# Optimization experiments

Measured on AMD Instinct MI355X. Metric: run time of the kernel, lower is better.

Reference implementation:

```python
import jax, jax.numpy as jnp
import numpy as np
from jax import lax

C_DIM = 64
N_HEADS = 8
PATCH = 3
PAD = (PATCH - 1) // 2
EPS = 1e-6


def _unfold(x, p, pad):
    # x: [B,C,H,W] -> [B, C*p*p, H*W], torch.F.unfold ordering (C slowest, then ph, pw)
    B, C, H, W = x.shape
    xp = jnp.pad(x, ((0, 0), (0, 0), (pad, pad), (pad, pad)))
    cols = jnp.stack([xp[:, :, i:i + H, j:j + W] for i in range(p) for j in range(p)], axis=2)
    return cols.reshape(B, C * p * p, H * W)


def _fold(cols, p, pad, H, W):
    # cols: [B, C*p*p, H*W] -> [B,C,H,W] via col2im scatter-add (torch.F.fold)
    B = cols.shape[0]
    C = cols.shape[1] // (p * p)
    cols = cols.reshape(B, C, p * p, H, W)
    out = jnp.zeros((B, C, H + 2 * pad, W + 2 * pad), cols.dtype)
    for i in range(p):
        for j in range(p):
            out = out.at[:, :, i:i + H, j:j + W].add(cols[:, :, i * p + j])
    return out[:, :, pad:pad + H, pad:pad + W]


def _linear_attn(q, k, v):
    # q,k,v: [B, h, N, d]; non-softmax linear attention with ReLU features
    kv = jnp.einsum('bhnd,bhne->bhde', k, v)          # [B,h,d,d]
    ksum = k.sum(axis=2)                              # [B,h,d]
    denom = jnp.einsum('bhnd,bhd->bhn', q, ksum) + EPS
    out = jnp.einsum('bhnd,bhde->bhne', q, kv) / denom[..., None]
    return out


def setup_inputs() -> dict:
    key = jax.random.key(0)
    ks = jax.random.split(key, 5)
    B, C, H, W = 4, C_DIM, 128, 128
    x = jax.random.normal(ks[0], (B, C, H, W), jnp.float32)
    w_qkv = jax.random.normal(ks[1], (3 * C, C), jnp.float32) * 0.05
    b_qkv = jax.random.normal(ks[2], (3 * C,), jnp.float32) * 0.01
    w_proj = jax.random.normal(ks[3], (C, C, 3, 3), jnp.float32) * 0.05
    b_proj = jax.random.normal(ks[4], (C,), jnp.float32) * 0.01
    return {"x": x, "w_qkv": w_qkv, "b_qkv": b_qkv, "w_proj": w_proj, "b_proj": b_proj}


def reference(x, w_qkv, b_qkv, w_proj, b_proj):
    B, C, H, W = x.shape
    p, pad, h = PATCH, PAD, N_HEADS
    N = H * W
    # 1x1 conv qkv
    qkv = jnp.einsum('bchw,oc->bohw', x, w_qkv) + b_qkv[None, :, None, None]
    q, k, v = qkv[:, :C], qkv[:, C:2 * C], qkv[:, 2 * C:]
    q = jax.nn.relu(q)
    k = jax.nn.relu(k)
    # im2col: [B, C*p*p, N]
    qc = _unfold(q, p, pad)
    kc = _unfold(k, p, pad)
    vc = _unfold(v, p, pad)
    d = (C * p * p) // h
    qh = qc.reshape(B, h, d, N).transpose(0, 1, 3, 2)  # [B,h,N,d]
    kh = kc.reshape(B, h, d, N).transpose(0, 1, 3, 2)
    vh = vc.reshape(B, h, d, N).transpose(0, 1, 3, 2)
    o = _linear_attn(qh, kh, vh)                       # [B,h,N,d]
    oc = o.transpose(0, 1, 3, 2).reshape(B, C * p * p, N)
    folded = _fold(oc, p, pad, H, W)
    ones_cols = _unfold(jnp.ones((B, C, H, W), x.dtype), p, pad)
    counts = _fold(ones_cols, p, pad, H, W)
    y = folded / counts
    # 3x3 proj conv
    y = lax.conv_general_dilated(y, w_proj, (1, 1), [(1, 1), (1, 1)],
                                 dimension_numbers=('NCHW', 'OIHW', 'NCHW'))
    y = y + b_proj[None, :, None, None]
    return y
```

## Files before the change

kernel.cpp:

```cpp
#include <hip/hip_runtime.h>

#define BB 4
#define CC 64
#define HH 128
#define WW 128
#define NN (HH*WW)
#define HP 130
#define NPP (HP*HP)
#define HP2 132
#define NPP2 (HP2*HP2)
#define NH 8
#define DD 72

__global__ __launch_bounds__(256) void k0_wt(const float* __restrict__ wproj, float* __restrict__ wt){
    int idx = blockIdx.x*256 + threadIdx.x;
    if (idx >= 64*9*64) return;
    int oc = idx & 63;
    int w  = (idx >> 6) % 9;
    int ci = idx / 576;
    wt[idx] = wproj[(oc*64 + ci)*9 + w];
}

__global__ __launch_bounds__(256) void k1_qkv(const float* __restrict__ x,
        const float* __restrict__ wqkv, const float* __restrict__ bqkv,
        float* __restrict__ Qp, float* __restrict__ Kp, float* __restrict__ Vp){
    __shared__ float wl[64*68];
    __shared__ float bl[64];
    const int t = threadIdx.x;
    const int gy = blockIdx.y;
    const int b  = blockIdx.z;
    for (int k = 0; k < 16; ++k){
        int idx = t + k*256;
        int orel = idx >> 6, c = idx & 63;
        wl[c*68 + orel] = wqkv[(gy*64 + orel)*64 + c];
    }
    if (t < 64) bl[t] = bqkv[gy*64 + t];
    __syncthreads();
    const int pix = blockIdx.x*256 + t;
    float acc[64];
#pragma unroll
    for (int o=0;o<64;++o) acc[o]=0.f;
    const float* xb = x + (size_t)(b*64)*NN + pix;
    for (int c=0;c<64;++c){
        float xv = xb[(size_t)c*NN];
        const float4* wrow = (const float4*)(&wl[c*68]);
#pragma unroll
        for (int o4=0;o4<16;++o4){
            float4 wv = wrow[o4];
            acc[o4*4+0] += xv*wv.x;
            acc[o4*4+1] += xv*wv.y;
            acc[o4*4+2] += xv*wv.z;
            acc[o4*4+3] += xv*wv.w;
        }
    }
    const int y = pix >> 7, xx = pix & 127;
    float* dst; size_t cstride;
    if (gy == 0){ dst = Qp + (size_t)(b*64)*NPP2 + (y+2)*HP2 + (xx+2); cstride = NPP2; }
    else { dst = ((gy==1)?Kp:Vp) + (size_t)(b*64)*NPP + (y+1)*HP + (xx+1); cstride = NPP; }
    const bool dorelu = (gy < 2);
#pragma unroll
    for (int o=0;o<64;++o){
        float v = acc[o] + bl[o];
        if (dorelu) v = fmaxf(v, 0.f);
        dst[(size_t)o*cstride] = v;
    }
}

__global__ __launch_bounds__(256) void k2_ksum(const float* __restrict__ Kp, float* __restrict__ ksum){
    const int c = blockIdx.x, b = blockIdx.y;
    const float* src = Kp + (size_t)(b*64 + c)*NPP;
    float a[3][3];
#pragma unroll
    for (int i=0;i<3;++i)
#pragma unroll
        for (int j=0;j<3;++j) a[i][j]=0.f;
    for (int idx = threadIdx.x; idx < NPP; idx += 256){
        int r = idx / HP, cc = idx - r*HP;
        float v = src[idx];
#pragma unroll
        for (int i=0;i<3;++i){
            bool fy = (unsigned)(r - i) < 128u;
#pragma unroll
            for (int j=0;j<3;++j){
                bool fx = (unsigned)(cc - j) < 128u;
                if (fy && fx) a[i][j] += v;
            }
        }
    }
    __shared__ float red[4][9];
#pragma unroll
    for (int i=0;i<3;++i)
#pragma unroll
        for (int j=0;j<3;++j){
            float v = a[i][j];
            for (int m=1;m<64;m<<=1) v += __shfl_xor(v, m, 64);
            a[i][j] = v;
        }
    int wave = threadIdx.x >> 6, lane = threadIdx.x & 63;
    if (lane == 0){
#pragma unroll
        for (int w=0;w<9;++w) red[wave][w] = a[w/3][w%3];
    }
    __syncthreads();
    if (threadIdx.x < 9){
        float s = red[0][threadIdx.x]+red[1][threadIdx.x]+red[2][threadIdx.x]+red[3][threadIdx.x];
        int h = c >> 3, cl = c & 7;
        ksum[(b*NH + h)*DD + cl*9 + threadIdx.x] = s;
    }
}

__global__ __launch_bounds__(256) void k3_kv(const float* __restrict__ Kp, const float* __restrict__ Vp,
                                             float* __restrict__ kvT2){
    const int cc2 = blockIdx.x;
    const int cd = cc2 >> 3, ce = cc2 & 7;
    const int h = blockIdx.y, b = blockIdx.z;
    const float* Kc = Kp + (size_t)(b*64 + h*8 + cd)*NPP;
    const float* Vc = Vp + (size_t)(b*64 + h*8 + ce)*NPP;
    float acc[9][9];
#pragma unroll
    for (int i=0;i<9;++i)
#pragma unroll
        for (int j=0;j<9;++j) acc[i][j]=0.f;
    for (int it=0; it<64; ++it){
        int pix = threadIdx.x + it*256;
        int y = pix >> 7, xx = pix & 127;
        const float* kb = Kc + y*HP + xx;
        const float* vb = Vc + y*HP + xx;
        float kw[9], vw[9];
#pragma unroll
        for (int w=0;w<9;++w){ kw[w] = kb[(w/3)*HP + (w%3)]; vw[w] = vb[(w/3)*HP + (w%3)]; }
#pragma unroll
        for (int w=0;w<9;++w)
#pragma unroll
            for (int w2=0;w2<9;++w2) acc[w][w2] += kw[w]*vw[w2];
    }
    __shared__ float red[4][81];
#pragma unroll
    for (int w=0;w<9;++w)
#pragma unroll
        for (int w2=0;w2<9;++w2){
            float v = acc[w][w2];
            for (int m=1;m<64;m<<=1) v += __shfl_xor(v, m, 64);
            acc[w][w2] = v;
        }
    int wave = threadIdx.x >> 6, lane = threadIdx.x & 63;
    if (lane == 0){
#pragma unroll
        for (int w=0;w<9;++w)
#pragma unroll
            for (int w2=0;w2<9;++w2) red[wave][w*9+w2] = acc[w][w2];
    }
    __syncthreads();
    if (threadIdx.x < 81){
        float s = red[0][threadIdx.x]+red[1][threadIdx.x]+red[2][threadIdx.x]+red[3][threadIdx.x];
        int w = threadIdx.x / 9, w2 = threadIdx.x - w*9;
        kvT2[((size_t)(b*NH + h)*DD + ce*9 + w2)*96 + cd*12 + w] = s;
    }
}

__global__ __launch_bounds__(256) void k4_r(const float* __restrict__ Qp, const float* __restrict__ ksum,
                                            float* __restrict__ rfp){
    const int h = blockIdx.y, b = blockIdx.z;
    __shared__ float ks[72];
    if (threadIdx.x < 72) ks[threadIdx.x] = ksum[(b*NH + h)*DD + threadIdx.x];
    __syncthreads();
    const int pix = blockIdx.x*256 + threadIdx.x;
    const int y = pix >> 7, xx = pix & 127;
    const float* Qb = Qp + (size_t)(b*64 + h*8)*NPP2 + (y+1)*HP2 + (xx+1);
    float denom = 0.f;
#pragma unroll
    for (int cl=0; cl<8; ++cl){
        const float* q = Qb + (size_t)cl*NPP2;
#pragma unroll
        for (int w=0; w<9; ++w){
            denom += q[(w/3)*HP2 + (w%3)] * ks[cl*9 + w];
        }
    }
    rfp[(size_t)(b*NH + h)*NPP + (y+1)*HP + (xx+1)] = 1.f/(denom + 1e-6f);
}

__global__ __launch_bounds__(512) void k5_attn(const float* __restrict__ Qp, const float* __restrict__ kvT2,
          const float* __restrict__ rfp, float* __restrict__ folded){
    __shared__ __align__(16) float Qt[8*20*20];
    __shared__ __align__(16) float rt[18*20];
    const int t = threadIdx.x;
    const int tile = blockIdx.x;
    const int h = blockIdx.y, b = blockIdx.z;
    const int ty0 = (tile >> 3)*16, tx0 = (tile & 7)*16;

    const float* Qb = Qp + (size_t)(b*64 + h*8)*NPP2 + (size_t)ty0*HP2 + tx0;
    for (int idx=t; idx<8*20*20; idx+=512){
        int cl = idx / 400; int rem = idx - cl*400; int r = rem/20, cc = rem - r*20;
        Qt[idx] = Qb[(size_t)cl*NPP2 + r*HP2 + cc];
    }
    const float* rg = rfp + (size_t)(b*NH + h)*NPP + (size_t)ty0*HP + tx0;
    for (int idx=t; idx<18*18; idx+=512){
        int rr = idx / 18, cc = idx - rr*18;
        rt[rr*20 + cc] = rg[rr*HP + cc];
    }
    __syncthreads();

    const int c  = __builtin_amdgcn_readfirstlane(t >> 6);
    const int l  = t & 63;
    const int pr = l >> 2;
    const int pc = (l & 3) * 4;

    const float* kvc = kvT2 + ((size_t)(b*NH + h)*DD + c*9)*96;

    float acc[9][4];
#pragma unroll
    for (int u=0;u<9;++u)
#pragma unroll
        for (int p=0;p<4;++p) acc[u][p]=0.f;

    for (int cl=0; cl<8; ++cl){
        float qw[5][8];
        const float* qb = &Qt[cl*400 + pr*20 + pc];
#pragma unroll
        for (int rr=0; rr<5; ++rr){
            float4 a0 = *(const float4*)(qb + rr*20);
            float4 a1 = *(const float4*)(qb + rr*20 + 4);
            qw[rr][0]=a0.x; qw[rr][1]=a0.y; qw[rr][2]=a0.z; qw[rr][3]=a0.w;
            qw[rr][4]=a1.x; qw[rr][5]=a1.y; qw[rr][6]=a1.z; qw[rr][7]=a1.w;
        }
#pragma unroll
        for (int u=0; u<9; ++u){
            const float* kr = kvc + u*96 + cl*12;
            float kw[9];
#pragma unroll
            for (int i=0;i<9;++i) kw[i] = kr[i];
            const int iu = u/3, ju = u - iu*3;
#pragma unroll
            for (int w=0; w<9; ++w){
                const int rr = (w/3) - iu + 2;
                const int cc = (w%3) - ju + 2;
#pragma unroll
                for (int p=0;p<4;++p)
                    acc[u][p] += qw[rr][cc+p] * kw[w];
            }
        }
    }
    float rw[3][6];
    const float* rb = &rt[pr*20 + pc];
#pragma unroll
    for (int rr=0; rr<3; ++rr)
#pragma unroll
        for (int j=0; j<6; ++j) rw[rr][j] = rb[rr*20 + j];
    float out[4];
#pragma unroll
    for (int p=0;p<4;++p) out[p]=0.f;
#pragma unroll
    for (int u=0; u<9; ++u){
        const int iu = u/3, ju = u - iu*3;
#pragma unroll
        for (int p=0;p<4;++p)
            out[p] += acc[u][p] * rw[2-iu][p+2-ju];
    }
    float4 o4 = make_float4(out[0], out[1], out[2], out[3]);
    *(float4*)(&folded[(size_t)(b*64 + h*8 + c)*NN + (ty0+pr)*WW + tx0 + pc]) = o4;
}

__global__ __launch_bounds__(256) void k6_conv(const float* __restrict__ folded, const float* __restrict__ wt,
         const float* __restrict__ bproj, float* __restrict__ out){
    __shared__ __align__(16) float ut[8*18*12];
    const int t = threadIdx.x;
    const int tile = blockIdx.x;
    const int b = blockIdx.y;
    const int ty0 = (tile >> 4)*16, tx0 = (tile & 15)*8;
    const int ocb = t & 15;
    const int s   = t >> 4;
    float acc[4][8];
#pragma unroll
    for (int ol=0;ol<4;++ol)
#pragma unroll
        for (int p=0;p<8;++p) acc[ol][p]=0.f;
    const float4 bias = *(const float4*)(&bproj[ocb*4]);

    for (int ch=0; ch<8; ++ch){
        __syncthreads();
        for (int idx=t; idx<8*18*10; idx+=256){
            int cil = idx / 180; int rem = idx - cil*180; int rr = rem/10, cc = rem - rr*10;
            int iy = ty0 - 1 + rr, ix = tx0 - 1 + cc;
            float v = 0.f;
            if ((unsigned)iy < 128u && (unsigned)ix < 128u){
                int ry = 3 - (iy==0) - (iy==127);
                int rx = 3 - (ix==0) - (ix==127);
                v = folded[(size_t)(b*64 + ch*8 + cil)*NN + iy*WW + ix] / (float)(ry*rx);
            }
            ut[cil*216 + rr*12 + cc] = v;
        }
        __syncthreads();
        for (int cil=0; cil<8; ++cil){
            const int ci = ch*8 + cil;
            float uw[3][10];
            const float* ub = &ut[cil*216 + s*12];
#pragma unroll
            for (int dy=0;dy<3;++dy){
                float4 a0 = *(const float4*)(ub + dy*12);
                float4 a1 = *(const float4*)(ub + dy*12 + 4);
                float2 a2 = *(const float2*)(ub + dy*12 + 8);
                uw[dy][0]=a0.x; uw[dy][1]=a0.y; uw[dy][2]=a0.z; uw[dy][3]=a0.w;
                uw[dy][4]=a1.x; uw[dy][5]=a1.y; uw[dy][6]=a1.z; uw[dy][7]=a1.w;
                uw[dy][8]=a2.x; uw[dy][9]=a2.y;
            }
#pragma unroll
            for (int w=0;w<9;++w){
                const int dy = w/3, dx = w%3;
                float4 wv = *(const float4*)(&wt[(ci*9 + w)*64 + ocb*4]);
#pragma unroll
                for (int p=0;p<8;++p){
                    float u = uw[dy][p+dx];
                    acc[0][p] += wv.x*u;
                    acc[1][p] += wv.y*u;
                    acc[2][p] += wv.z*u;
                    acc[3][p] += wv.w*u;
                }
            }
        }
    }
    const int y = ty0 + s;
#pragma unroll
    for (int ol=0;ol<4;++ol){
        const int oc = ocb*4 + ol;
        float* dst = &out[(size_t)(b*64 + oc)*NN + y*WW + tx0];
        float bv = (ol==0)?bias.x:(ol==1)?bias.y:(ol==2)?bias.z:bias.w;
#pragma unroll
        for (int p=0;p<8;++p) dst[p] = acc[ol][p] + bv;
    }
}

extern "C" void kernel_launch(void* const* d_in, const int* in_sizes, int n_in,
                              void* d_out, int out_size, void* d_ws, size_t ws_size,
                              hipStream_t stream) {
    const float* x     = (const float*)d_in[0];
    const float* wqkv  = (const float*)d_in[1];
    const float* bqkv  = (const float*)d_in[2];
    const float* wproj = (const float*)d_in[3];
    const float* bproj = (const float*)d_in[4];
    float* out = (float*)d_out;
    float* ws  = (float*)d_ws;

    const size_t szQ2 = (size_t)BB*CC*NPP2;
    const size_t szF  = (size_t)BB*CC*NPP;
    const size_t szR  = (size_t)BB*NH*NPP;
    float* Qp2    = ws;
    float* Kp     = Qp2 + szQ2;
    float* Vp     = Kp + szF;
    float* rfp    = Vp + szF;
    float* folded = rfp + szR;
    float* kvT2   = folded + (size_t)BB*CC*NN;
    float* ksum   = kvT2 + (size_t)BB*NH*DD*96;
    float* wt     = ksum + (size_t)BB*NH*DD;

    hipMemsetAsync(ws, 0, (szQ2 + 2*szF + szR)*sizeof(float), stream);

    k0_wt  <<<dim3(144),      256, 0, stream>>>(wproj, wt);
    k1_qkv <<<dim3(64, 3, 4), 256, 0, stream>>>(x, wqkv, bqkv, Qp2, Kp, Vp);
    k2_ksum<<<dim3(64, 4),    256, 0, stream>>>(Kp, ksum);
    k3_kv  <<<dim3(64, 8, 4), 256, 0, stream>>>(Kp, Vp, kvT2);
    k4_r   <<<dim3(64, 8, 4), 256, 0, stream>>>(Qp2, ksum, rfp);
    k5_attn<<<dim3(64, 8, 4), 512, 0, stream>>>(Qp2, kvT2, rfp, folded);
    k6_conv<<<dim3(128, 4),   256, 0, stream>>>(folded, wt, bproj, out);
}
```

Before: 416.5 us.

## Fuse ksum into KV kernel with LDS-tiled 72x72 outer product and atomic reduction

Replaces the per-channel-pair KV kernel and the separate ksum kernel with one kernel. Each block stages a strip of pixels for all 72 unfolded K and V features of a head in LDS, and each thread computes a 9x9 tile of the 72x72 KV matrix. This removes the 64-fold redundant global reads of K and V across channel pairs and the costly shuffle reductions. The ksum accumulation rides along on a subset of lanes. Partial results across spatial blocks are combined with global atomicAdd into buffers that are now zeroed by the memset, which adds atomic traffic and makes the summation order nondeterministic.

Measured after the change: 695.0 us. 66.9% more time.

```diff
diff --git a/kernel.cpp b/kernel.cpp
--- a/kernel.cpp
+++ b/kernel.cpp
@@ -66,95 +66,106 @@
     }
 }
 
-__global__ __launch_bounds__(256) void k2_ksum(const float* __restrict__ Kp, float* __restrict__ ksum){
-    const int c = blockIdx.x, b = blockIdx.y;
-    const float* src = Kp + (size_t)(b*64 + c)*NPP;
-    float a[3][3];
-#pragma unroll
-    for (int i=0;i<3;++i)
-#pragma unroll
-        for (int j=0;j<3;++j) a[i][j]=0.f;
-    for (int idx = threadIdx.x; idx < NPP; idx += 256){
-        int r = idx / HP, cc = idx - r*HP;
-        float v = src[idx];
-#pragma unroll
-        for (int i=0;i<3;++i){
-            bool fy = (unsigned)(r - i) < 128u;
-#pragma unroll
-            for (int j=0;j<3;++j){
-                bool fx = (unsigned)(cc - j) < 128u;
-                if (fy && fx) a[i][j] += v;
-            }
-        }
-    }
-    __shared__ float red[4][9];
-#pragma unroll
-    for (int i=0;i<3;++i)
-#pragma unroll
-        for (int j=0;j<3;++j){
-            float v = a[i][j];
-            for (int m=1;m<64;m<<=1) v += __shfl_xor(v, m, 64);
-            a[i][j] = v;
-        }
-    int wave = threadIdx.x >> 6, lane = threadIdx.x & 63;
-    if (lane == 0){
-#pragma unroll
-        for (int w=0;w<9;++w) red[wave][w] = a[w/3][w%3];
+__global__ __launch_bounds__(256) void k3_kv(const float* __restrict__ Kp, const float* __restrict__ Vp,
+                                             float* __restrict__ kvT2, float* __restrict__ ksum){
+    __shared__ __align__(16) float lds[2*72*68];
+    float* Kt = lds;
+    float* Vt = lds + 72*68;
+    const int t = threadIdx.x;
+    const int h = blockIdx.y, b = blockIdx.z;
+    const int y0 = blockIdx.x * 4;
+    const int bh = b*NH + h;
+    const float* Kb = Kp + (size_t)(b*64 + h*8)*NPP;
+    const float* Vb = Vp + (size_t)(b*64 + h*8)*NPP;
+
+    const int p  = t & 63;
+    const int d0 = t >> 6;
+    const int lbase = d0*68 + p;
+    int ofs[18];
+#pragma unroll
+    for (int k=0;k<18;++k){
+        int d = d0 + 4*k;
+        int cl = d/9, w = d - 9*cl, wi = w/3, wj = w - 3*wi;
+        ofs[k] = cl*NPP + wi*HP + wj + p;
+    }
+
+    const int l  = t & 63;
+    const int i9 = (l >> 3) * 9;
+    const int j9 = (l & 7) * 9;
+    const bool ks_lane = ((l & 7) == 0);
+
+    float acc[9][9];
+#pragma unroll
+    for (int a=0;a<9;++a)
+#pragma unroll
+        for (int c=0;c<9;++c) acc[a][c]=0.f;
+    float ksa[9];
+#pragma unroll
+    for (int a=0;a<9;++a) ksa[a]=0.f;
+
+    for (int r = 0; r < 8; ++r){
+        const int y  = y0 + (r >> 1);
+        const int x0 = (r & 1) * 64;
+        const int gof = y*HP + x0;
+        __syncthreads();
+#pragma unroll
+        for (int k=0;k<18;++k){
+            Kt[lbase + 272*k] = Kb[ofs[k] + gof];
+            Vt[lbase + 272*k] = Vb[ofs[k] + gof];
+        }
+        __syncthreads();
+        const int p0 = (t >> 6) * 16;
+#pragma unroll
+        for (int g=0; g<4; ++g){
+            float4 kf[9];
+            const float* kb2 = &Kt[i9*68 + p0 + 4*g];
+#pragma unroll
+            for (int a=0;a<9;++a) kf[a] = *(const float4*)(kb2 + a*68);
+            if (ks_lane){
+#pragma unroll
+                for (int a=0;a<9;++a) ksa[a] += kf[a].x+kf[a].y+kf[a].z+kf[a].w;
+            }
+            const float* vb2 = &Vt[j9*68 + p0 + 4*g];
+#pragma unroll
+            for (int c3=0;c3<3;++c3){
+                float4 vf[3];
+#pragma unroll
+                for (int cc=0;cc<3;++cc) vf[cc] = *(const float4*)(vb2 + (c3*3+cc)*68);
+#pragma unroll
+                for (int a=0;a<9;++a)
+#pragma unroll
+                    for (int cc=0;cc<3;++cc){
+                        acc[a][c3*3+cc] += kf[a].x*vf[cc].x + kf[a].y*vf[cc].y
+                                         + kf[a].z*vf[cc].z + kf[a].w*vf[cc].w;
+                    }
+            }
+        }
     }
     __syncthreads();
-    if (threadIdx.x < 9){
-        float s = red[0][threadIdx.x]+red[1][threadIdx.x]+red[2][threadIdx.x]+red[3][threadIdx.x];
-        int h = c >> 3, cl = c & 7;
-        ksum[(b*NH + h)*DD + cl*9 + threadIdx.x] = s;
-    }
-}
-
-__global__ __launch_bounds__(256) void k3_kv(const float* __restrict__ Kp, const float* __restrict__ Vp,
-                                             float* __restrict__ kvT2){
-    const int cc2 = blockIdx.x;
-    const int cd = cc2 >> 3, ce = cc2 & 7;
-    const int h = blockIdx.y, b = blockIdx.z;
-    const float* Kc = Kp + (size_t)(b*64 + h*8 + cd)*NPP;
-    const float* Vc = Vp + (size_t)(b*64 + h*8 + ce)*NPP;
-    float acc[9][9];
-#pragma unroll
-    for (int i=0;i<9;++i)
-#pragma unroll
-        for (int j=0;j<9;++j) acc[i][j]=0.f;
-    for (int it=0; it<64; ++it){
-        int pix = threadIdx.x + it*256;
-        int y = pix >> 7, xx = pix & 127;
-        const float* kb = Kc + y*HP + xx;
-        const float* vb = Vc + y*HP + xx;
-        float kw[9], vw[9];
-#pragma unroll
-        for (int w=0;w<9;++w){ kw[w] = kb[(w/3)*HP + (w%3)]; vw[w] = vb[(w/3)*HP + (w%3)]; }
-#pragma unroll
-        for (int w=0;w<9;++w)
-#pragma unroll
-            for (int w2=0;w2<9;++w2) acc[w][w2] += kw[w]*vw[w2];
-    }
-    __shared__ float red[4][81];
-#pragma unroll
-    for (int w=0;w<9;++w)
-#pragma unroll
-        for (int w2=0;w2<9;++w2){
-            float v = acc[w][w2];
-            for (int m=1;m<64;m<<=1) v += __shfl_xor(v, m, 64);
-            acc[w][w2] = v;
-        }
-    int wave = threadIdx.x >> 6, lane = threadIdx.x & 63;
-    if (lane == 0){
-#pragma unroll
-        for (int w=0;w<9;++w)
-#pragma unroll
-            for (int w2=0;w2<9;++w2) red[wave][w*9+w2] = acc[w][w2];
-    }
-    __syncthreads();
-    if (threadIdx.x < 81){
-        float s = red[0][threadIdx.x]+red[1][threadIdx.x]+red[2][threadIdx.x]+red[3][threadIdx.x];
-        int w = threadIdx.x / 9, w2 = threadIdx.x - w*9;
-        kvT2[((size_t)(b*NH + h)*DD + ce*9 + w2)*96 + cd*12 + w] = s;
+    const int wv = t >> 6;
+    for (int turn=0; turn<4; ++turn){
+        if (wv == turn){
+#pragma unroll
+            for (int a=0;a<9;++a)
+#pragma unroll
+                for (int c=0;c<9;++c){
+                    float* cell = &lds[(i9+a)*72 + (j9+c)];
+                    if (turn == 0) *cell = acc[a][c];
+                    else           *cell += acc[a][c];
+                }
+        }
+        __syncthreads();
+    }
+    float* kvdst = kvT2 + (size_t)bh*DD*96;
+    for (int idx=t; idx<72*72; idx+=256){
+        int e = idx / 72, d = idx - e*72;
+        int cd = d / 9, w = d - cd*9;
+        atomicAdd(&kvdst[e*96 + cd*12 + w], lds[d*72 + e]);
+    }
+    if (ks_lane){
+        float* kd = ksum + (size_t)bh*DD;
+#pragma unroll
+        for (int a=0;a<9;++a) atomicAdd(&kd[i9+a], ksa[a]);
     }
 }
 
@@ -343,21 +354,22 @@
     const size_t szQ2 = (size_t)BB*CC*NPP2;
     const size_t szF  = (size_t)BB*CC*NPP;
     const size_t szR  = (size_t)BB*NH*NPP;
+    const size_t szKV = (size_t)BB*NH*DD*96;
+    const size_t szKS = (size_t)BB*NH*DD;
     float* Qp2    = ws;
     float* Kp     = Qp2 + szQ2;
     float* Vp     = Kp + szF;
     float* rfp    = Vp + szF;
-    float* folded = rfp + szR;
-    float* kvT2   = folded + (size_t)BB*CC*NN;
-    float* ksum   = kvT2 + (size_t)BB*NH*DD*96;
-    float* wt     = ksum + (size_t)BB*NH*DD;
-
-    hipMemsetAsync(ws, 0, (szQ2 + 2*szF + szR)*sizeof(float), stream);
+    float* kvT2   = rfp + szR;
+    float* ksum   = kvT2 + szKV;
+    float* folded = ksum + szKS;
+    float* wt     = folded + (size_t)BB*CC*NN;
+
+    hipMemsetAsync(ws, 0, (szQ2 + 2*szF + szR + szKV + szKS)*sizeof(float), stream);
 
     k0_wt  <<<dim3(144),      256, 0, stream>>>(wproj, wt);
     k1_qkv <<<dim3(64, 3, 4), 256, 0, stream>>>(x, wqkv, bqkv, Qp2, Kp, Vp);
-    k2_ksum<<<dim3(64, 4),    256, 0, stream>>>(Kp, ksum);
-    k3_kv  <<<dim3(64, 8, 4), 256, 0, stream>>>(Kp, Vp, kvT2);
+    k3_kv  <<<dim3(32, 8, 4), 256, 0, stream>>>(Kp, Vp, kvT2, ksum);
     k4_r   <<<dim3(64, 8, 4), 256, 0, stream>>>(Qp2, ksum, rfp);
     k5_attn<<<dim3(64, 8, 4), 512, 0, stream>>>(Qp2, kvT2, rfp, folded);
     k6_conv<<<dim3(128, 4),   256, 0, stream>>>(folded, wt, bproj, out);
```

## Pad K/V row stride to 132 and register-tile k3_kv over 4-pixel strips

Applied to the files above, without the earlier changes.

The K and V buffers now use a row stride of 132 floats instead of 130, so each row starts 16-byte aligned. k3_kv has each thread load a 3x8 window of K and V with float4 loads and reuse it across 4 adjacent pixels. This replaces 18 scalar gathers per pixel and is meant to cut load instruction count and redundant memory traffic in the K^T V accumulation. The producer kernel, the ksum kernel and the workspace layout are updated to match. The cost is slightly larger buffers and a bigger memset, and k2_ksum now also reads the unused padding columns.

After: 429.7 us. +3.2%, slower.

```diff
diff --git a/kernel.cpp b/kernel.cpp
--- a/kernel.cpp
+++ b/kernel.cpp
@@ -7,6 +7,8 @@
 #define NN (HH*WW)
 #define HP 130
 #define NPP (HP*HP)
+#define HPS 132
+#define NPPS (130*HPS)
 #define HP2 132
 #define NPP2 (HP2*HP2)
 #define NH 8
@@ -56,7 +58,7 @@
     const int y = pix >> 7, xx = pix & 127;
     float* dst; size_t cstride;
     if (gy == 0){ dst = Qp + (size_t)(b*64)*NPP2 + (y+2)*HP2 + (xx+2); cstride = NPP2; }
-    else { dst = ((gy==1)?Kp:Vp) + (size_t)(b*64)*NPP + (y+1)*HP + (xx+1); cstride = NPP; }
+    else { dst = ((gy==1)?Kp:Vp) + (size_t)(b*64)*NPPS + (y+1)*HPS + (xx+1); cstride = NPPS; }
     const bool dorelu = (gy < 2);
 #pragma unroll
     for (int o=0;o<64;++o){
@@ -68,14 +70,14 @@
 
 __global__ __launch_bounds__(256) void k2_ksum(const float* __restrict__ Kp, float* __restrict__ ksum){
     const int c = blockIdx.x, b = blockIdx.y;
-    const float* src = Kp + (size_t)(b*64 + c)*NPP;
+    const float* src = Kp + (size_t)(b*64 + c)*NPPS;
     float a[3][3];
 #pragma unroll
     for (int i=0;i<3;++i)
 #pragma unroll
         for (int j=0;j<3;++j) a[i][j]=0.f;
-    for (int idx = threadIdx.x; idx < NPP; idx += 256){
-        int r = idx / HP, cc = idx - r*HP;
+    for (int idx = threadIdx.x; idx < NPPS; idx += 256){
+        int r = idx / HPS, cc = idx - r*HPS;
         float v = src[idx];
 #pragma unroll
         for (int i=0;i<3;++i){
@@ -114,25 +116,42 @@
     const int cc2 = blockIdx.x;
     const int cd = cc2 >> 3, ce = cc2 & 7;
     const int h = blockIdx.y, b = blockIdx.z;
-    const float* Kc = Kp + (size_t)(b*64 + h*8 + cd)*NPP;
-    const float* Vc = Vp + (size_t)(b*64 + h*8 + ce)*NPP;
+    const float* Kc = Kp + (size_t)(b*64 + h*8 + cd)*NPPS;
+    const float* Vc = Vp + (size_t)(b*64 + h*8 + ce)*NPPS;
+    const int x0 = (threadIdx.x & 31) * 4;
+    const int yb = threadIdx.x >> 5;
     float acc[9][9];
 #pragma unroll
     for (int i=0;i<9;++i)
 #pragma unroll
         for (int j=0;j<9;++j) acc[i][j]=0.f;
-    for (int it=0; it<64; ++it){
-        int pix = threadIdx.x + it*256;
-        int y = pix >> 7, xx = pix & 127;
-        const float* kb = Kc + y*HP + xx;
-        const float* vb = Vc + y*HP + xx;
-        float kw[9], vw[9];
-#pragma unroll
-        for (int w=0;w<9;++w){ kw[w] = kb[(w/3)*HP + (w%3)]; vw[w] = vb[(w/3)*HP + (w%3)]; }
-#pragma unroll
-        for (int w=0;w<9;++w)
-#pragma unroll
-            for (int w2=0;w2<9;++w2) acc[w][w2] += kw[w]*vw[w2];
+
+    for (int it=0; it<16; ++it){
+        const int y = it*8 + yb;
+        const float* kb = Kc + y*HPS + x0;
+        const float* vb = Vc + y*HPS + x0;
+        float kr[3][8], vr[3][8];
+#pragma unroll
+        for (int rr=0; rr<3; ++rr){
+            float4 a0 = *(const float4*)(kb + rr*HPS);
+            float4 a1 = *(const float4*)(kb + rr*HPS + 4);
+            kr[rr][0]=a0.x; kr[rr][1]=a0.y; kr[rr][2]=a0.z; kr[rr][3]=a0.w;
+            kr[rr][4]=a1.x; kr[rr][5]=a1.y; kr[rr][6]=a1.z; kr[rr][7]=a1.w;
+            float4 b0 = *(const float4*)(vb + rr*HPS);
+            float4 b1 = *(const float4*)(vb + rr*HPS + 4);
+            vr[rr][0]=b0.x; vr[rr][1]=b0.y; vr[rr][2]=b0.z; vr[rr][3]=b0.w;
+            vr[rr][4]=b1.x; vr[rr][5]=b1.y; vr[rr][6]=b1.z; vr[rr][7]=b1.w;
+        }
+#pragma unroll
+        for (int p=0; p<4; ++p){
+#pragma unroll
+            for (int w=0; w<9; ++w){
+                const float kv_ = kr[w/3][p + (w%3)];
+#pragma unroll
+                for (int w2=0; w2<9; ++w2)
+                    acc[w][w2] += kv_ * vr[w2/3][p + (w2%3)];
+            }
+        }
     }
     __shared__ float red[4][81];
 #pragma unroll
@@ -341,18 +360,20 @@
     float* ws  = (float*)d_ws;
 
     const size_t szQ2 = (size_t)BB*CC*NPP2;
-    const size_t szF  = (size_t)BB*CC*NPP;
+    const size_t szFS = (size_t)BB*CC*NPPS;
     const size_t szR  = (size_t)BB*NH*NPP;
+    const size_t szKV = (size_t)BB*NH*DD*96;
+    const size_t szKS = (size_t)BB*NH*DD;
     float* Qp2    = ws;
     float* Kp     = Qp2 + szQ2;
-    float* Vp     = Kp + szF;
-    float* rfp    = Vp + szF;
-    float* folded = rfp + szR;
-    float* kvT2   = folded + (size_t)BB*CC*NN;
-    float* ksum   = kvT2 + (size_t)BB*NH*DD*96;
-    float* wt     = ksum + (size_t)BB*NH*DD;
-
-    hipMemsetAsync(ws, 0, (szQ2 + 2*szF + szR)*sizeof(float), stream);
+    float* Vp     = Kp + szFS;
+    float* rfp    = Vp + szFS;
+    float* kvT2   = rfp + szR;
+    float* ksum   = kvT2 + szKV;
+    float* folded = ksum + szKS;
+    float* wt     = folded + (size_t)BB*CC*NN;
+
+    hipMemsetAsync(ws, 0, (szQ2 + 2*szFS + szR)*sizeof(float), stream);
 
     k0_wt  <<<dim3(144),      256, 0, stream>>>(wproj, wt);
     k1_qkv <<<dim3(64, 3, 4), 256, 0, stream>>>(x, wqkv, bqkv, Qp2, Kp, Vp);
```
